# Kernel optimization log

Hardware: AMD Instinct MI355X
Metric: run time of the kernel (lower is better)

## Reference

```python
import jax, jax.numpy as jnp
import numpy as np

N = 50000   # total residue nodes across the batch of peptides
E = 800000  # total directed intra-peptide edges (avg degree 16)
D = 512


def _w(k, shape):
    fan_in = shape[0]
    return (jax.random.normal(k, shape, jnp.float32) / np.sqrt(fan_in)).astype(jnp.float32)


def setup_inputs() -> dict:
    key = jax.random.key(0)
    ks = jax.random.split(key, 12)
    return {
        "peptide_feature": jax.random.normal(ks[0], (N, D), jnp.float32),
        "edge_index": jax.random.randint(ks[1], (2, E), 0, N),
        # aanet_proj: 512 -> 1024 -> 1024 -> 512 -> 80 (ReLU between, none after last)
        "W1": _w(ks[2], (512, 1024)), "b1": jnp.zeros((1024,), jnp.float32),
        "W2": _w(ks[3], (1024, 1024)), "b2": jnp.zeros((1024,), jnp.float32),
        "W3": _w(ks[4], (1024, 512)), "b3": jnp.zeros((512,), jnp.float32),
        "W4": _w(ks[5], (512, 80)), "b4": jnp.zeros((80,), jnp.float32),
        # in_net: 80 -> 512
        "Win": _w(ks[6], (80, 512)), "bin_": jnp.zeros((512,), jnp.float32),
        # GIN conv MLP: 512 -> 512 -> 512 (eps = 0)
        "Wg1": _w(ks[7], (512, 512)), "bg1": jnp.zeros((512,), jnp.float32),
        "Wg2": _w(ks[8], (512, 512)), "bg2": jnp.zeros((512,), jnp.float32),
        # out_net: 512 -> 80
        "Wout": _w(ks[9], (512, 80)), "bout": jnp.zeros((80,), jnp.float32),
    }


def reference(peptide_feature, edge_index, W1, b1, W2, b2, W3, b3, W4, b4,
              Win, bin_, Wg1, bg1, Wg2, bg2, Wout, bout):
    relu = jax.nn.relu
    # aanet_proj
    h = relu(peptide_feature @ W1 + b1)
    h = relu(h @ W2 + b2)
    h = relu(h @ W3 + b3)
    peptide_feat = h @ W4 + b4                      # [N, 80]
    # in_net
    x = peptide_feat @ Win + bin_                   # [N, 512]
    # GIN message passing (sum aggregation, eps=0): per-sample loop in the
    # original is equivalent to one global pass since edges are sample-local.
    src, dst = edge_index[0], edge_index[1]
    agg = jax.ops.segment_sum(x[src], dst, num_segments=N)   # [N, 512]
    g = x + agg
    g = relu(g @ Wg1 + bg1) @ Wg2 + bg2             # GIN MLP
    # out_net
    peptide_mask = g @ Wout + bout                  # [N, 80]
    return peptide_mask, peptide_feat
```

## Files before the change

### kernel.cpp

```cpp
#include <hip/hip_runtime.h>
#include <stdint.h>


using bf16x8 = __attribute__((ext_vector_type(8))) short;
using f32x4  = __attribute__((ext_vector_type(4))) float;

__device__ inline unsigned short f2bf(float f) {
    union { float f; unsigned u; } v; v.f = f;
    unsigned u = v.u;
    u += 0x7FFFu + ((u >> 16) & 1u);
    return (unsigned short)(u >> 16);
}
__device__ inline float bf2f(unsigned u16) {
    return __uint_as_float(u16 << 16);
}

struct PreDescs {
    const float* W[8]; unsigned short* Wt[8];
    int K[8], M[8], Kp[8], ntx[8], start[8];
    int tEnd, cEnd, eEnd;
    const float* feat; unsigned short* featb; int nFeat;
    const int* ei; int E; int* cnt;
};

__global__ __launch_bounds__(256) void rg_preprocess(PreDescs d) {
    int b = blockIdx.x;
    int tid = threadIdx.x;
    if (b < d.tEnd) {
        __shared__ float t[32][33];
        int di = 0;
#pragma unroll
        for (int i = 1; i < 8; ++i) if (b >= d.start[i]) di = i;
        int local = b - d.start[di];
        int bx = local % d.ntx[di];
        int by = local / d.ntx[di];
        const float* W = d.W[di];
        unsigned short* Wt = d.Wt[di];
        int K = d.K[di], M = d.M[di], Kp = d.Kp[di];
        int mb = bx * 32, kb = by * 32;
        int tx = tid & 31, tg = tid >> 5;
#pragma unroll
        for (int p = 0; p < 4; ++p) {
            int r = tg + p * 8;
            int k = kb + r, m = mb + tx;
            t[r][tx] = (k < K && m < M) ? W[(size_t)k * M + m] : 0.f;
        }
        __syncthreads();
#pragma unroll
        for (int p = 0; p < 4; ++p) {
            int r = tg + p * 8;
            int mo = mb + r, ko = kb + tx;
            Wt[(size_t)mo * Kp + ko] = f2bf(t[tx][r]);
        }
    } else if (b < d.cEnd) {
        int i = ((b - d.tEnd) * 256 + tid) * 4;
        if (i + 3 < d.nFeat) {
            float4 v = *(const float4*)(d.feat + i);
            ushort4 o; o.x = f2bf(v.x); o.y = f2bf(v.y); o.z = f2bf(v.z); o.w = f2bf(v.w);
            *(ushort4*)(d.featb + i) = o;
        }
    } else {
        int e = (b - d.cEnd) * 256 + tid;
        if (e < d.E) atomicAdd(&d.cnt[d.ei[d.E + e]], 1);
    }
}

template <bool RELU, bool OUT_BF, bool OUT_F32, bool DEGB, int MT>
__global__ __launch_bounds__(256) void rg_gemm(
    const unsigned short* __restrict__ A, const unsigned short* __restrict__ Bt,
    const float* __restrict__ bias, const int* __restrict__ deg, int Mvalid,
    unsigned short* __restrict__ outB, float* __restrict__ outF,
    int Nrows, int Kp, int Mp, int gN)
{
    __shared__ __align__(16) unsigned short As[128 * 64];
    __shared__ __align__(16) unsigned short Bs[128 * 64];

    int bid = blockIdx.x;
    int xcd = bid & 7;
    int slot = bid >> 3;
    int c = slot % MT;
    int rsub = slot / MT;
    int rt = rsub * 8 + xcd;
    if (rt >= gN) return;
    const int rowBase = rt * 128;
    const int nBase   = c * 128;

    const int tid  = threadIdx.x;
    const int lane = tid & 63;
    const int w    = tid >> 6;
    const int wm   = w & 1, wn = w >> 1;

    f32x4 acc[4][4];
#pragma unroll
    for (int i = 0; i < 4; ++i)
#pragma unroll
        for (int j = 0; j < 4; ++j) acc[i][j] = (f32x4){0.f, 0.f, 0.f, 0.f};

    const int nkt = Kp >> 6;
    for (int kt = 0; kt < nkt; ++kt) {
        __syncthreads();
        const int k0 = kt * 64;
#pragma unroll
        for (int i = 0; i < 4; ++i) {
            int q   = i * 256 + tid;
            int r   = q >> 3;
            int cbg = (q & 7) ^ (r & 7);
            const unsigned short* gp = A + (size_t)(rowBase + r) * Kp + k0 + cbg * 8;
            __builtin_amdgcn_global_load_lds(
                (const __attribute__((address_space(1))) void*)gp,
                (__attribute__((address_space(3))) void*)(&As[q * 8]), 16, 0, 0);
        }
#pragma unroll
        for (int i = 0; i < 4; ++i) {
            int q   = i * 256 + tid;
            int r   = q >> 3;
            int cbg = (q & 7) ^ (r & 7);
            const unsigned short* gp = Bt + (size_t)(nBase + r) * Kp + k0 + cbg * 8;
            __builtin_amdgcn_global_load_lds(
                (const __attribute__((address_space(1))) void*)gp,
                (__attribute__((address_space(3))) void*)(&Bs[q * 8]), 16, 0, 0);
        }
        __syncthreads();
#pragma unroll
        for (int kk = 0; kk < 2; ++kk) {
            bf16x8 a[4], b[4];
            const int cb = kk * 4 + (lane >> 4);
#pragma unroll
            for (int i = 0; i < 4; ++i) {
                int r = wm * 64 + i * 16 + (lane & 15);
                a[i] = *(const bf16x8*)&As[(r * 8 + (cb ^ (r & 7))) * 8];
            }
#pragma unroll
            for (int j = 0; j < 4; ++j) {
                int r = wn * 64 + j * 16 + (lane & 15);
                b[j] = *(const bf16x8*)&Bs[(r * 8 + (cb ^ (r & 7))) * 8];
            }
#pragma unroll
            for (int i = 0; i < 4; ++i)
#pragma unroll
                for (int j = 0; j < 4; ++j)
                    acc[i][j] = __builtin_amdgcn_mfma_f32_16x16x32_bf16(b[j], a[i], acc[i][j], 0, 0, 0);
        }
    }

    const int quad = lane >> 4;
#pragma unroll
    for (int i = 0; i < 4; ++i) {
        int row = rowBase + wm * 64 + i * 16 + (lane & 15);
        if (row >= Nrows) continue;
        float sc = 1.f;
        if (DEGB) sc = 1.f + (float)deg[row];
#pragma unroll
        for (int j = 0; j < 4; ++j) {
            int colb = nBase + wn * 64 + j * 16 + quad * 4;
            float4 bv = (colb < Mvalid) ? *(const float4*)(bias + colb)
                                        : (float4){0.f, 0.f, 0.f, 0.f};
            float v0 = acc[i][j][0] + sc * bv.x;
            float v1 = acc[i][j][1] + sc * bv.y;
            float v2 = acc[i][j][2] + sc * bv.z;
            float v3 = acc[i][j][3] + sc * bv.w;
            if (RELU) {
                v0 = v0 > 0.f ? v0 : 0.f; v1 = v1 > 0.f ? v1 : 0.f;
                v2 = v2 > 0.f ? v2 : 0.f; v3 = v3 > 0.f ? v3 : 0.f;
            }
            if (OUT_BF) {
                ushort4 o; o.x = f2bf(v0); o.y = f2bf(v1); o.z = f2bf(v2); o.w = f2bf(v3);
                *(ushort4*)(outB + (size_t)row * Mp + colb) = o;
            }
            if (OUT_F32) {
                if (colb < Mvalid)
                    *(float4*)(outF + (size_t)row * Mvalid + colb) = (float4){v0, v1, v2, v3};
            }
        }
    }
}

__global__ void rg_scan_block(const int* __restrict__ cnt, int* __restrict__ scanned,
                              int* __restrict__ bsums, int Nn) {
    __shared__ int sd[1024];
    int tid = threadIdx.x;
    int i = blockIdx.x * 1024 + tid;
    int v = (i < Nn) ? cnt[i] : 0;
    sd[tid] = v;
    __syncthreads();
    for (int off = 1; off < 1024; off <<= 1) {
        int t = (tid >= off) ? sd[tid - off] : 0;
        __syncthreads();
        sd[tid] += t;
        __syncthreads();
    }
    if (i < Nn) scanned[i] = sd[tid];
    if (tid == 1023) bsums[blockIdx.x] = sd[1023];
}

__global__ void rg_scan_sums(int* __restrict__ b, int nb) {
    int tid = threadIdx.x;
    int carry = 0;
    for (int base = 0; base < nb; base += 64) {
        int i = base + tid;
        int v = (i < nb) ? b[i] : 0;
        int incl = v;
#pragma unroll
        for (int off = 1; off < 64; off <<= 1) {
            int t = __shfl_up(incl, off, 64);
            if (tid >= off) incl += t;
        }
        if (i < nb) b[i] = carry + incl - v;
        carry += __shfl(incl, 63, 64);
    }
}

__global__ void rg_scan_add(const int* __restrict__ scanned, const int* __restrict__ bsums,
                            const int* __restrict__ cnt, int* __restrict__ rowptr,
                            int* __restrict__ cursor, int Nn, int E) {
    int i = blockIdx.x * 1024 + threadIdx.x;
    if (i < Nn) {
        int ex = scanned[i] - cnt[i] + bsums[blockIdx.x];
        rowptr[i] = ex; cursor[i] = ex;
    }
    if (i == 0) rowptr[Nn] = E;
}

__global__ void rg_scatter_edges(const int* __restrict__ ei, int E,
                                 int* __restrict__ cursor, int* __restrict__ cols) {
    int e = blockIdx.x * 256 + threadIdx.x;
    if (e < E) {
        int d = ei[E + e];
        int p = atomicAdd(&cursor[d], 1);
        cols[p] = ei[e];
    }
}

__global__ __launch_bounds__(256) void rg_agg80(
    const unsigned short* __restrict__ pf, const int* __restrict__ rowptr,
    const int* __restrict__ cols, unsigned short* __restrict__ s, int Nn)
{
    int node = blockIdx.x * 4 + (threadIdx.x >> 6);
    if (node >= Nn) return;
    int lane = threadIdx.x & 63;
    const unsigned* xp = (const unsigned*)pf;
    size_t off = (size_t)node * 64 + lane;
    unsigned u = xp[off];
    float a0 = bf2f(u & 0xffffu), a1 = bf2f(u >> 16);
    int beg = rowptr[node], end = rowptr[node + 1];
    int e = beg;
    for (; e + 8 <= end; e += 8) {
        unsigned v[8];
#pragma unroll
        for (int t = 0; t < 8; ++t) v[t] = xp[(size_t)cols[e + t] * 64 + lane];
#pragma unroll
        for (int t = 0; t < 8; ++t) { a0 += bf2f(v[t] & 0xffffu); a1 += bf2f(v[t] >> 16); }
    }
    for (; e < end; ++e) {
        unsigned v = xp[(size_t)cols[e] * 64 + lane];
        a0 += bf2f(v & 0xffffu); a1 += bf2f(v >> 16);
    }
    unsigned o = (unsigned)f2bf(a0) | ((unsigned)f2bf(a1) << 16);
    ((unsigned*)s)[off] = o;
}

extern "C" void kernel_launch(void* const* d_in, const int* in_sizes, int n_in,
                              void* d_out, int out_size, void* d_ws, size_t ws_size,
                              hipStream_t stream)
{
    const float* feat = (const float*)d_in[0];
    const int*   ei   = (const int*)d_in[1];
    const float* W1 = (const float*)d_in[2];  const float* b1 = (const float*)d_in[3];
    const float* W2 = (const float*)d_in[4];  const float* b2 = (const float*)d_in[5];
    const float* W3 = (const float*)d_in[6];  const float* b3 = (const float*)d_in[7];
    const float* W4 = (const float*)d_in[8];  const float* b4 = (const float*)d_in[9];
    const float* Wi = (const float*)d_in[10]; const float* bi = (const float*)d_in[11];
    const float* Wg1 = (const float*)d_in[12]; const float* bg1 = (const float*)d_in[13];
    const float* Wg2 = (const float*)d_in[14]; const float* bg2 = (const float*)d_in[15];
    const float* Wo = (const float*)d_in[16]; const float* bo = (const float*)d_in[17];

    const int N = in_sizes[0] / 512;
    const int E = in_sizes[1] / 2;
    const int gN = (N + 127) / 128;
    const int Npad = gN * 128;

    char* ws = (char*)d_ws;
    size_t o = 0;
    auto alloc = [&](size_t bytes) { char* p = ws + o; o += (bytes + 255) & ~(size_t)255; return p; };
    unsigned short* bufA = (unsigned short*)alloc((size_t)Npad * 1024 * 2);
    unsigned short* bufB = (unsigned short*)alloc((size_t)Npad * 1024 * 2);
    unsigned short* bufC = (unsigned short*)alloc((size_t)Npad * 512 * 2);
    unsigned short* W1t = (unsigned short*)alloc((size_t)1024 * 512 * 2);
    unsigned short* W2t = (unsigned short*)alloc((size_t)1024 * 1024 * 2);
    unsigned short* W3t = (unsigned short*)alloc((size_t)512 * 1024 * 2);
    unsigned short* W4t = (unsigned short*)alloc((size_t)128 * 512 * 2);
    unsigned short* Wit = (unsigned short*)alloc((size_t)512 * 128 * 2);
    unsigned short* Wg1t = (unsigned short*)alloc((size_t)512 * 512 * 2);
    unsigned short* Wg2t = (unsigned short*)alloc((size_t)512 * 512 * 2);
    unsigned short* Wot = (unsigned short*)alloc((size_t)128 * 512 * 2);
    int* cnt    = (int*)alloc((size_t)N * 4);
    int* rowptr = (int*)alloc((size_t)(N + 1) * 4);
    int* cursor = (int*)alloc((size_t)N * 4);
    int* cols   = (int*)alloc((size_t)E * 4);
    int* bsums  = (int*)alloc(256);

    float* out_mask = (float*)d_out;
    float* out_feat = (float*)d_out + (size_t)N * 80;

    hipMemsetAsync(cnt, 0, (size_t)N * 4, stream);
    {
        PreDescs d;
        const float* Ws[8]  = {W1, W2, W3, W4, Wi, Wg1, Wg2, Wo};
        unsigned short* Ts[8] = {W1t, W2t, W3t, W4t, Wit, Wg1t, Wg2t, Wot};
        int Ks[8]  = {512, 1024, 1024, 512, 80, 512, 512, 512};
        int Ms[8]  = {1024, 1024, 512, 80, 512, 512, 512, 80};
        int Kps[8] = {512, 1024, 1024, 512, 128, 512, 512, 512};
        int Mps[8] = {1024, 1024, 512, 128, 512, 512, 512, 128};
        int st = 0;
        for (int i = 0; i < 8; ++i) {
            d.W[i] = Ws[i]; d.Wt[i] = Ts[i];
            d.K[i] = Ks[i]; d.M[i] = Ms[i]; d.Kp[i] = Kps[i];
            d.ntx[i] = Mps[i] / 32;
            d.start[i] = st;
            st += (Mps[i] / 32) * (Kps[i] / 32);
        }
        d.tEnd = st;
        d.cEnd = st + (N * 512) / 1024;
        d.eEnd = d.cEnd + (E + 255) / 256;
        d.feat = feat; d.featb = bufC; d.nFeat = N * 512;
        d.ei = ei; d.E = E; d.cnt = cnt;
        rg_preprocess<<<d.eEnd, 256, 0, stream>>>(d);
    }

    int* scanned = cols;
    const int nb = (N + 1023) / 1024;
    rg_scan_block<<<nb, 1024, 0, stream>>>(cnt, scanned, bsums, N);
    rg_scan_sums<<<1, 64, 0, stream>>>(bsums, nb);
    rg_scan_add<<<nb, 1024, 0, stream>>>(scanned, bsums, cnt, rowptr, cursor, N, E);
    rg_scatter_edges<<<(E + 255) / 256, 256, 0, stream>>>(ei, E, cursor, cols);

    const int rg8 = ((gN + 7) / 8) * 8;
    auto grid = [&](int MT) { return dim3(rg8 * MT); };

    rg_gemm<true, true, false, false, 8><<<grid(8), 256, 0, stream>>>(bufC, W1t, b1, nullptr, 1024, bufA, nullptr, N, 512, 1024, gN);
    rg_gemm<true, true, false, false, 8><<<grid(8), 256, 0, stream>>>(bufA, W2t, b2, nullptr, 1024, bufB, nullptr, N, 1024, 1024, gN);
    rg_gemm<true, true, false, false, 4><<<grid(4), 256, 0, stream>>>(bufB, W3t, b3, nullptr, 512, bufC, nullptr, N, 1024, 512, gN);
    rg_gemm<false, true, true, false, 1><<<grid(1), 256, 0, stream>>>(bufC, W4t, b4, nullptr, 80, bufA, out_feat, N, 512, 128, gN);

    rg_agg80<<<(N + 3) / 4, 256, 0, stream>>>(bufA, rowptr, cols, bufC, N);

    rg_gemm<false, true, false, true, 4><<<grid(4), 256, 0, stream>>>(bufC, Wit, bi, cnt, 512, bufA, nullptr, N, 128, 512, gN);
    rg_gemm<true, true, false, false, 4><<<grid(4), 256, 0, stream>>>(bufA, Wg1t, bg1, nullptr, 512, bufB, nullptr, N, 512, 512, gN);
    rg_gemm<false, true, false, false, 4><<<grid(4), 256, 0, stream>>>(bufB, Wg2t, bg2, nullptr, 512, bufC, nullptr, N, 512, 512, gN);
    rg_gemm<false, false, true, false, 1><<<grid(1), 256, 0, stream>>>(bufC, Wot, bo, nullptr, 80, nullptr, out_mask, N, 512, 128, gN);
}
```

Before: 816.0 us.

## Fuse CSR build into one grid-barrier kernel and use 64-row tiles for narrow GEMMs

Replaces the memset, the degree-count branch of preprocess and four separate scan and scatter launches with a single persistent kernel. That kernel uses a software grid barrier across its 49 blocks of 1024 threads, cutting launch overhead and serial kernel gaps. It also adds a 64-row tile variant of the GEMM for the two narrow 512-to-80 projections, doubling their block count to improve occupancy across CUs. The grid barrier assumes all blocks are co-resident, and the CSR now runs serially before preprocess instead of overlapping with its weight-transpose work.

```diff
diff --git a/kernel.cpp b/kernel.cpp
--- a/kernel.cpp
+++ b/kernel.cpp
@@ -18,9 +18,8 @@
 struct PreDescs {
     const float* W[8]; unsigned short* Wt[8];
     int K[8], M[8], Kp[8], ntx[8], start[8];
-    int tEnd, cEnd, eEnd;
+    int tEnd, cEnd;
     const float* feat; unsigned short* featb; int nFeat;
-    const int* ei; int E; int* cnt;
 };
 
 __global__ __launch_bounds__(256) void rg_preprocess(PreDescs d) {
@@ -52,27 +51,92 @@
             int mo = mb + r, ko = kb + tx;
             Wt[(size_t)mo * Kp + ko] = f2bf(t[tx][r]);
         }
-    } else if (b < d.cEnd) {
+    } else {
         int i = ((b - d.tEnd) * 256 + tid) * 4;
         if (i + 3 < d.nFeat) {
             float4 v = *(const float4*)(d.feat + i);
             ushort4 o; o.x = f2bf(v.x); o.y = f2bf(v.y); o.z = f2bf(v.z); o.w = f2bf(v.w);
             *(ushort4*)(d.featb + i) = o;
         }
-    } else {
-        int e = (b - d.cEnd) * 256 + tid;
-        if (e < d.E) atomicAdd(&d.cnt[d.ei[d.E + e]], 1);
-    }
-}
-
-template <bool RELU, bool OUT_BF, bool OUT_F32, bool DEGB, int MT>
+    }
+}
+
+__device__ __forceinline__ void rg_gridbar(int* bar, int nb, int phase) {
+    __syncthreads();
+    if (threadIdx.x == 0) {
+        __threadfence();
+        atomicAdd(bar, 1);
+        int target = phase * nb;
+        while (__hip_atomic_load(bar, __ATOMIC_RELAXED, __HIP_MEMORY_SCOPE_AGENT) < target) {}
+        __threadfence();
+    }
+    __syncthreads();
+}
+
+__global__ __launch_bounds__(1024) void rg_csr(
+    const int* __restrict__ ei, int E, int Nn,
+    int* __restrict__ cnt, int* __restrict__ rowptr, int* __restrict__ cursor,
+    int* __restrict__ cols, int* __restrict__ bsums, int* bar, int nb)
+{
+    __shared__ int sd[1024];
+    const int tid  = threadIdx.x;
+    const int bid  = blockIdx.x;
+    const int gsz  = nb * 1024;
+    const int gtid = bid * 1024 + tid;
+
+    for (int i = gtid; i < Nn; i += gsz) cnt[i] = 0;
+    rg_gridbar(bar, nb, 1);
+
+    for (int e = gtid; e < E; e += gsz) atomicAdd(&cnt[ei[E + e]], 1);
+    rg_gridbar(bar, nb, 2);
+
+    int i = gtid;
+    int v = (i < Nn) ? cnt[i] : 0;
+    sd[tid] = v;
+    __syncthreads();
+    for (int off = 1; off < 1024; off <<= 1) {
+        int t = (tid >= off) ? sd[tid - off] : 0;
+        __syncthreads();
+        sd[tid] += t;
+        __syncthreads();
+    }
+    if (tid == 1023) bsums[bid] = sd[1023];
+    rg_gridbar(bar, nb, 3);
+
+    if (bid == 0 && tid < 64) {
+        int bv = (tid < nb) ? bsums[tid] : 0;
+        int incl = bv;
+#pragma unroll
+        for (int off = 1; off < 64; off <<= 1) {
+            int t = __shfl_up(incl, off, 64);
+            if (tid >= off) incl += t;
+        }
+        if (tid < nb) bsums[tid] = incl - bv;
+    }
+    rg_gridbar(bar, nb, 4);
+
+    if (i < Nn) {
+        int ex = sd[tid] - v + bsums[bid];
+        rowptr[i] = ex; cursor[i] = ex;
+    }
+    if (gtid == 0) rowptr[Nn] = E;
+    rg_gridbar(bar, nb, 5);
+
+    for (int e = gtid; e < E; e += gsz) {
+        int d = ei[E + e];
+        int p = atomicAdd(&cursor[d], 1);
+        cols[p] = ei[e];
+    }
+}
+
+template <bool RELU, bool OUT_BF, bool OUT_F32, bool DEGB, int MT, int ROWS>
 __global__ __launch_bounds__(256) void rg_gemm(
     const unsigned short* __restrict__ A, const unsigned short* __restrict__ Bt,
     const float* __restrict__ bias, const int* __restrict__ deg, int Mvalid,
     unsigned short* __restrict__ outB, float* __restrict__ outF,
     int Nrows, int Kp, int Mp, int gN)
 {
-    __shared__ __align__(16) unsigned short As[128 * 64];
+    __shared__ __align__(16) unsigned short As[ROWS * 64];
     __shared__ __align__(16) unsigned short Bs[128 * 64];
 
     int bid = blockIdx.x;
@@ -82,26 +146,30 @@
     int rsub = slot / MT;
     int rt = rsub * 8 + xcd;
     if (rt >= gN) return;
-    const int rowBase = rt * 128;
+    const int rowBase = rt * ROWS;
     const int nBase   = c * 128;
 
     const int tid  = threadIdx.x;
     const int lane = tid & 63;
     const int w    = tid >> 6;
-    const int wm   = w & 1, wn = w >> 1;
-
-    f32x4 acc[4][4];
+    constexpr int CJ = (ROWS == 128) ? 4 : 2;
+    const int wm = (ROWS == 128) ? (w & 1) : 0;
+    const int wn = (ROWS == 128) ? (w >> 1) : w;
+    const int rowOffW = wm * 64;
+    const int colOffW = wn * ((ROWS == 128) ? 64 : 32);
+
+    f32x4 acc[4][CJ];
 #pragma unroll
     for (int i = 0; i < 4; ++i)
 #pragma unroll
-        for (int j = 0; j < 4; ++j) acc[i][j] = (f32x4){0.f, 0.f, 0.f, 0.f};
+        for (int j = 0; j < CJ; ++j) acc[i][j] = (f32x4){0.f, 0.f, 0.f, 0.f};
 
     const int nkt = Kp >> 6;
     for (int kt = 0; kt < nkt; ++kt) {
         __syncthreads();
         const int k0 = kt * 64;
 #pragma unroll
-        for (int i = 0; i < 4; ++i) {
+        for (int i = 0; i < ROWS * 8 / 256; ++i) {
             int q   = i * 256 + tid;
             int r   = q >> 3;
             int cbg = (q & 7) ^ (r & 7);
@@ -123,22 +191,22 @@
         __syncthreads();
 #pragma unroll
         for (int kk = 0; kk < 2; ++kk) {
-            bf16x8 a[4], b[4];
+            bf16x8 a[4], b[CJ];
             const int cb = kk * 4 + (lane >> 4);
 #pragma unroll
             for (int i = 0; i < 4; ++i) {
-                int r = wm * 64 + i * 16 + (lane & 15);
+                int r = rowOffW + i * 16 + (lane & 15);
                 a[i] = *(const bf16x8*)&As[(r * 8 + (cb ^ (r & 7))) * 8];
             }
 #pragma unroll
-            for (int j = 0; j < 4; ++j) {
-                int r = wn * 64 + j * 16 + (lane & 15);
+            for (int j = 0; j < CJ; ++j) {
+                int r = colOffW + j * 16 + (lane & 15);
                 b[j] = *(const bf16x8*)&Bs[(r * 8 + (cb ^ (r & 7))) * 8];
             }
 #pragma unroll
             for (int i = 0; i < 4; ++i)
 #pragma unroll
-                for (int j = 0; j < 4; ++j)
+                for (int j = 0; j < CJ; ++j)
                     acc[i][j] = __builtin_amdgcn_mfma_f32_16x16x32_bf16(b[j], a[i], acc[i][j], 0, 0, 0);
         }
     }
@@ -146,13 +214,13 @@
     const int quad = lane >> 4;
 #pragma unroll
     for (int i = 0; i < 4; ++i) {
-        int row = rowBase + wm * 64 + i * 16 + (lane & 15);
+        int row = rowBase + rowOffW + i * 16 + (lane & 15);
         if (row >= Nrows) continue;
         float sc = 1.f;
         if (DEGB) sc = 1.f + (float)deg[row];
 #pragma unroll
-        for (int j = 0; j < 4; ++j) {
-            int colb = nBase + wn * 64 + j * 16 + quad * 4;
+        for (int j = 0; j < CJ; ++j) {
+            int colb = nBase + colOffW + j * 16 + quad * 4;
             float4 bv = (colb < Mvalid) ? *(const float4*)(bias + colb)
                                         : (float4){0.f, 0.f, 0.f, 0.f};
             float v0 = acc[i][j][0] + sc * bv.x;
@@ -172,62 +240,6 @@
                     *(float4*)(outF + (size_t)row * Mvalid + colb) = (float4){v0, v1, v2, v3};
             }
         }
-    }
-}
-
-__global__ void rg_scan_block(const int* __restrict__ cnt, int* __restrict__ scanned,
-                              int* __restrict__ bsums, int Nn) {
-    __shared__ int sd[1024];
-    int tid = threadIdx.x;
-    int i = blockIdx.x * 1024 + tid;
-    int v = (i < Nn) ? cnt[i] : 0;
-    sd[tid] = v;
-    __syncthreads();
-    for (int off = 1; off < 1024; off <<= 1) {
-        int t = (tid >= off) ? sd[tid - off] : 0;
-        __syncthreads();
-        sd[tid] += t;
-        __syncthreads();
-    }
-    if (i < Nn) scanned[i] = sd[tid];
-    if (tid == 1023) bsums[blockIdx.x] = sd[1023];
-}
-
-__global__ void rg_scan_sums(int* __restrict__ b, int nb) {
-    int tid = threadIdx.x;
-    int carry = 0;
-    for (int base = 0; base < nb; base += 64) {
-        int i = base + tid;
-        int v = (i < nb) ? b[i] : 0;
-        int incl = v;
-#pragma unroll
-        for (int off = 1; off < 64; off <<= 1) {
-            int t = __shfl_up(incl, off, 64);
-            if (tid >= off) incl += t;
-        }
-        if (i < nb) b[i] = carry + incl - v;
-        carry += __shfl(incl, 63, 64);
-    }
-}
-
-__global__ void rg_scan_add(const int* __restrict__ scanned, const int* __restrict__ bsums,
-                            const int* __restrict__ cnt, int* __restrict__ rowptr,
-                            int* __restrict__ cursor, int Nn, int E) {
-    int i = blockIdx.x * 1024 + threadIdx.x;
-    if (i < Nn) {
-        int ex = scanned[i] - cnt[i] + bsums[blockIdx.x];
-        rowptr[i] = ex; cursor[i] = ex;
-    }
-    if (i == 0) rowptr[Nn] = E;
-}
-
-__global__ void rg_scatter_edges(const int* __restrict__ ei, int E,
-                                 int* __restrict__ cursor, int* __restrict__ cols) {
-    int e = blockIdx.x * 256 + threadIdx.x;
-    if (e < E) {
-        int d = ei[E + e];
-        int p = atomicAdd(&cursor[d], 1);
-        cols[p] = ei[e];
     }
 }
 
@@ -278,6 +290,7 @@
     const int E = in_sizes[1] / 2;
     const int gN = (N + 127) / 128;
     const int Npad = gN * 128;
+    const int gN64 = Npad / 64;
 
     char* ws = (char*)d_ws;
     size_t o = 0;
@@ -298,11 +311,15 @@
     int* cursor = (int*)alloc((size_t)N * 4);
     int* cols   = (int*)alloc((size_t)E * 4);
     int* bsums  = (int*)alloc(256);
+    int* bar    = (int*)alloc(256);
 
     float* out_mask = (float*)d_out;
     float* out_feat = (float*)d_out + (size_t)N * 80;
 
-    hipMemsetAsync(cnt, 0, (size_t)N * 4, stream);
+    hipMemsetAsync(bar, 0, 16, stream);
+    const int nb = (N + 1023) / 1024;
+    rg_csr<<<nb, 1024, 0, stream>>>(ei, E, N, cnt, rowptr, cursor, cols, bsums, bar, nb);
+
     {
         PreDescs d;
         const float* Ws[8]  = {W1, W2, W3, W4, Wi, Wg1, Wg2, Wo};
@@ -321,31 +338,23 @@
         }
         d.tEnd = st;
         d.cEnd = st + (N * 512) / 1024;
-        d.eEnd = d.cEnd + (E + 255) / 256;
         d.feat = feat; d.featb = bufC; d.nFeat = N * 512;
-        d.ei = ei; d.E = E; d.cnt = cnt;
-        rg_preprocess<<<d.eEnd, 256, 0, stream>>>(d);
-    }
-
-    int* scanned = cols;
-    const int nb = (N + 1023) / 1024;
-    rg_scan_block<<<nb, 1024, 0, stream>>>(cnt, scanned, bsums, N);
-    rg_scan_sums<<<1, 64, 0, stream>>>(bsums, nb);
-    rg_scan_add<<<nb, 1024, 0, stream>>>(scanned, bsums, cnt, rowptr, cursor, N, E);
-    rg_scatter_edges<<<(E + 255) / 256, 256, 0, stream>>>(ei, E, cursor, cols);
-
-    const int rg8 = ((gN + 7) / 8) * 8;
+        rg_preprocess<<<d.cEnd, 256, 0, stream>>>(d);
+    }
+
+    const int rg8   = ((gN + 7) / 8) * 8;
+    const int rg864 = ((gN64 + 7) / 8) * 8;
     auto grid = [&](int MT) { return dim3(rg8 * MT); };
 
-    rg_gemm<true, true, false, false, 8><<<grid(8), 256, 0, stream>>>(bufC, W1t, b1, nullptr, 1024, bufA, nullptr, N, 512, 1024, gN);
-    rg_gemm<true, true, false, false, 8><<<grid(8), 256, 0, stream>>>(bufA, W2t, b2, nullptr, 1024, bufB, nullptr, N, 1024, 1024, gN);
-    rg_gemm<true, true, false, false, 4><<<grid(4), 256, 0, stream>>>(bufB, W3t, b3, nullptr, 512, bufC, nullptr, N, 1024, 512, gN);
-    rg_gemm<false, true, true, false, 1><<<grid(1), 256, 0, stream>>>(bufC, W4t, b4, nullptr, 80, bufA, out_feat, N, 512, 128, gN);
+    rg_gemm<true, true, false, false, 8, 128><<<grid(8), 256, 0, stream>>>(bufC, W1t, b1, nullptr, 1024, bufA, nullptr, N, 512, 1024, gN);
+    rg_gemm<true, true, false, false, 8, 128><<<grid(8), 256, 0, stream>>>(bufA, W2t, b2, nullptr, 1024, bufB, nullptr, N, 1024, 1024, gN);
+    rg_gemm<true, true, false, false, 4, 128><<<grid(4), 256, 0, stream>>>(bufB, W3t, b3, nullptr, 512, bufC, nullptr, N, 1024, 512, gN);
+    rg_gemm<false, true, true, false, 1, 64><<<dim3(rg864), 256, 0, stream>>>(bufC, W4t, b4, nullptr, 80, bufA, out_feat, N, 512, 128, gN64);
 
     rg_agg80<<<(N + 3) / 4, 256, 0, stream>>>(bufA, rowptr, cols, bufC, N);
 
-    rg_gemm<false, true, false, true, 4><<<grid(4), 256, 0, stream>>>(bufC, Wit, bi, cnt, 512, bufA, nullptr, N, 128, 512, gN);
-    rg_gemm<true, true, false, false, 4><<<grid(4), 256, 0, stream>>>(bufA, Wg1t, bg1, nullptr, 512, bufB, nullptr, N, 512, 512, gN);
-    rg_gemm<false, true, false, false, 4><<<grid(4), 256, 0, stream>>>(bufB, Wg2t, bg2, nullptr, 512, bufC, nullptr, N, 512, 512, gN);
-    rg_gemm<false, false, true, false, 1><<<grid(1), 256, 0, stream>>>(bufC, Wot, bo, nullptr, 80, nullptr, out_mask, N, 512, 128, gN);
-}
+    rg_gemm<false, true, false, true, 4, 128><<<grid(4), 256, 0, stream>>>(bufC, Wit, bi, cnt, 512, bufA, nullptr, N, 128, 512, gN);
+    rg_gemm<true, true, false, false, 4, 128><<<grid(4), 256, 0, stream>>>(bufA, Wg1t, bg1, nullptr, 512, bufB, nullptr, N, 512, 512, gN);
+    rg_gemm<false, true, false, false, 4, 128><<<grid(4), 256, 0, stream>>>(bufB, Wg2t, bg2, nullptr, 512, bufC, nullptr, N, 512, 512, gN);
+    rg_gemm<false, false, true, false, 1, 64><<<dim3(rg864), 256, 0, stream>>>(bufC, Wot, bo, nullptr, 80, nullptr, out_mask, N, 512, 128, gN64);
+}
```

After: 835.4 us. 1.02x slower.

## Fuse three scan kernels with a grid barrier; split W2 GEMM into halves

Applied to the files above, without the earlier changes.

Replaces the three-kernel prefix scan (block scan, block-sum scan, add) with one kernel that uses a spin-wait grid barrier on an atomic counter placed after the count array. This removes two launches and a round trip through global memory. It also splits the 1024x1024 W2 GEMM into two launches over the two halves of the rows. The grid barrier relies on all 49 blocks of 1024 threads being co-resident, which could deadlock otherwise.

```diff
diff --git a/kernel.cpp b/kernel.cpp
--- a/kernel.cpp
+++ b/kernel.cpp
@@ -175,11 +175,27 @@
     }
 }
 
-__global__ void rg_scan_block(const int* __restrict__ cnt, int* __restrict__ scanned,
-                              int* __restrict__ bsums, int Nn) {
+__device__ __forceinline__ void rg_gridbar(int* bar, int nb, int phase) {
+    __syncthreads();
+    if (threadIdx.x == 0) {
+        __threadfence();
+        atomicAdd(bar, 1);
+        int target = phase * nb;
+        while (__hip_atomic_load(bar, __ATOMIC_RELAXED, __HIP_MEMORY_SCOPE_AGENT) < target) {}
+        __threadfence();
+    }
+    __syncthreads();
+}
+
+__global__ __launch_bounds__(1024) void rg_scan_all(
+    const int* __restrict__ cnt, int* __restrict__ rowptr, int* __restrict__ cursor,
+    int* __restrict__ bsums, int* bar, int Nn, int E, int nb)
+{
     __shared__ int sd[1024];
-    int tid = threadIdx.x;
-    int i = blockIdx.x * 1024 + tid;
+    const int tid = threadIdx.x;
+    const int bid = blockIdx.x;
+    const int i   = bid * 1024 + tid;
+
     int v = (i < Nn) ? cnt[i] : 0;
     sd[tid] = v;
     __syncthreads();
@@ -189,33 +205,23 @@
         sd[tid] += t;
         __syncthreads();
     }
-    if (i < Nn) scanned[i] = sd[tid];
-    if (tid == 1023) bsums[blockIdx.x] = sd[1023];
-}
-
-__global__ void rg_scan_sums(int* __restrict__ b, int nb) {
-    int tid = threadIdx.x;
-    int carry = 0;
-    for (int base = 0; base < nb; base += 64) {
-        int i = base + tid;
-        int v = (i < nb) ? b[i] : 0;
-        int incl = v;
+    if (tid == 1023) bsums[bid] = sd[1023];
+    rg_gridbar(bar, nb, 1);
+
+    if (bid == 0 && tid < 64) {
+        int bv = (tid < nb) ? bsums[tid] : 0;
+        int incl = bv;
 #pragma unroll
         for (int off = 1; off < 64; off <<= 1) {
             int t = __shfl_up(incl, off, 64);
             if (tid >= off) incl += t;
         }
-        if (i < nb) b[i] = carry + incl - v;
-        carry += __shfl(incl, 63, 64);
-    }
-}
-
-__global__ void rg_scan_add(const int* __restrict__ scanned, const int* __restrict__ bsums,
-                            const int* __restrict__ cnt, int* __restrict__ rowptr,
-                            int* __restrict__ cursor, int Nn, int E) {
-    int i = blockIdx.x * 1024 + threadIdx.x;
+        if (tid < nb) bsums[tid] = incl - bv;
+    }
+    rg_gridbar(bar, nb, 2);
+
     if (i < Nn) {
-        int ex = scanned[i] - cnt[i] + bsums[blockIdx.x];
+        int ex = sd[tid] - v + bsums[bid];
         rowptr[i] = ex; cursor[i] = ex;
     }
     if (i == 0) rowptr[Nn] = E;
@@ -293,7 +299,8 @@
     unsigned short* Wg1t = (unsigned short*)alloc((size_t)512 * 512 * 2);
     unsigned short* Wg2t = (unsigned short*)alloc((size_t)512 * 512 * 2);
     unsigned short* Wot = (unsigned short*)alloc((size_t)128 * 512 * 2);
-    int* cnt    = (int*)alloc((size_t)N * 4);
+    int* cnt    = (int*)alloc((size_t)(N + 64) * 4);
+    int* bar    = cnt + N;
     int* rowptr = (int*)alloc((size_t)(N + 1) * 4);
     int* cursor = (int*)alloc((size_t)N * 4);
     int* cols   = (int*)alloc((size_t)E * 4);
@@ -302,7 +309,7 @@
     float* out_mask = (float*)d_out;
     float* out_feat = (float*)d_out + (size_t)N * 80;
 
-    hipMemsetAsync(cnt, 0, (size_t)N * 4, stream);
+    hipMemsetAsync(cnt, 0, (size_t)(N + 64) * 4, stream);
     {
         PreDescs d;
         const float* Ws[8]  = {W1, W2, W3, W4, Wi, Wg1, Wg2, Wo};
@@ -327,18 +334,28 @@
         rg_preprocess<<<d.eEnd, 256, 0, stream>>>(d);
     }
 
-    int* scanned = cols;
     const int nb = (N + 1023) / 1024;
-    rg_scan_block<<<nb, 1024, 0, stream>>>(cnt, scanned, bsums, N);
-    rg_scan_sums<<<1, 64, 0, stream>>>(bsums, nb);
-    rg_scan_add<<<nb, 1024, 0, stream>>>(scanned, bsums, cnt, rowptr, cursor, N, E);
+    rg_scan_all<<<nb, 1024, 0, stream>>>(cnt, rowptr, cursor, bsums, bar, N, E, nb);
     rg_scatter_edges<<<(E + 255) / 256, 256, 0, stream>>>(ei, E, cursor, cols);
 
     const int rg8 = ((gN + 7) / 8) * 8;
     auto grid = [&](int MT) { return dim3(rg8 * MT); };
 
     rg_gemm<true, true, false, false, 8><<<grid(8), 256, 0, stream>>>(bufC, W1t, b1, nullptr, 1024, bufA, nullptr, N, 512, 1024, gN);
-    rg_gemm<true, true, false, false, 8><<<grid(8), 256, 0, stream>>>(bufA, W2t, b2, nullptr, 1024, bufB, nullptr, N, 1024, 1024, gN);
+
+    {
+        const int halfTiles = (gN + 1) / 2;
+        const int halfRows  = halfTiles * 128;
+        const int gNb       = gN - halfTiles;
+        const int rg8a = ((halfTiles + 7) / 8) * 8;
+        const int rg8b = ((gNb + 7) / 8) * 8;
+        rg_gemm<true, true, false, false, 8><<<dim3(rg8a * 8), 256, 0, stream>>>(
+            bufA, W2t, b2, nullptr, 1024, bufB, nullptr, halfRows, 1024, 1024, halfTiles);
+        rg_gemm<true, true, false, false, 8><<<dim3(rg8b * 8), 256, 0, stream>>>(
+            bufA + (size_t)halfRows * 1024, W2t, b2, nullptr, 1024,
+            bufB + (size_t)halfRows * 1024, nullptr, N - halfRows, 1024, 1024, gNb);
+    }
+
     rg_gemm<true, true, false, false, 4><<<grid(4), 256, 0, stream>>>(bufB, W3t, b3, nullptr, 512, bufC, nullptr, N, 1024, 512, gN);
     rg_gemm<false, true, true, false, 1><<<grid(1), 256, 0, stream>>>(bufC, W4t, b4, nullptr, 80, bufA, out_feat, N, 512, 128, gN);
 
```

New measurement: 848.4 us. 4.0% more time.
